# Performance work log

Measured on AMD Instinct MI355X. Metric: run time of the kernel, lower is better.

## Reference

```python
import jax, jax.numpy as jnp
import numpy as np

DIM = 384
HEADS = 8
ADLA = 343
HWD = 14
N = HWD ** 3
B = 8
HEAD_DIM = DIM // HEADS
SCALE = HEAD_DIM ** -0.5
POOL = 7  # ceil(343**(1/3)); 14 is evenly divisible by 7


def _lin_mat(in_size, out_size):
    # PyTorch trilinear interpolation (align_corners=False), one axis -> (out,in) matrix
    scale = in_size / out_size
    x = (np.arange(out_size) + 0.5) * scale - 0.5
    x = np.clip(x, 0.0, in_size - 1)
    x0 = np.floor(x).astype(np.int64)
    x1 = np.minimum(x0 + 1, in_size - 1)
    w = (x - x0).astype(np.float32)
    M = np.zeros((out_size, in_size), np.float32)
    M[np.arange(out_size), x0] += 1.0 - w
    M[np.arange(out_size), x1] += w
    return jnp.asarray(M)


def _interp3(t, out_hwd):
    # t: (..., a, b, c) -> (..., H, W, D) trilinear, align_corners=False
    Ma = _lin_mat(t.shape[-3], out_hwd[0])
    Mb = _lin_mat(t.shape[-2], out_hwd[1])
    Mc = _lin_mat(t.shape[-1], out_hwd[2])
    return jnp.einsum('...abc,xa,yb,zc->...xyz', t, Ma, Mb, Mc)


def setup_inputs() -> dict:
    key = jax.random.key(0)
    ks = jax.random.split(key, 16)
    std = 0.02
    return {
        'x': jax.random.normal(ks[0], (B, N, DIM), jnp.float32),
        'Wq': jax.random.normal(ks[1], (DIM, DIM), jnp.float32) * std,
        'Wkv': jax.random.normal(ks[2], (DIM, 2 * DIM), jnp.float32) * std,
        'Wproj': jax.random.normal(ks[3], (DIM, DIM), jnp.float32) * std,
        'bproj': jnp.zeros((DIM,), jnp.float32),
        'dwc_w': jax.random.normal(ks[4], (DIM, 1, 3, 3, 3), jnp.float32) * std,
        'dwc_b': jnp.zeros((DIM,), jnp.float32),
        'an_bias': jax.random.normal(ks[5], (HEADS, ADLA, 7, 7, 7), jnp.float32) * std,
        'na_bias': jax.random.normal(ks[6], (HEADS, ADLA, 7, 7, 7), jnp.float32) * std,
        'ah_bias': jax.random.normal(ks[7], (1, HEADS, ADLA, HWD, 1, 1), jnp.float32) * std,
        'aw_bias': jax.random.normal(ks[8], (1, HEADS, ADLA, 1, HWD, 1), jnp.float32) * std,
        'ad_bias': jax.random.normal(ks[9], (1, HEADS, ADLA, 1, 1, HWD), jnp.float32) * std,
        'ha_bias': jax.random.normal(ks[10], (1, HEADS, HWD, 1, 1, ADLA), jnp.float32) * std,
        'wa_bias': jax.random.normal(ks[11], (1, HEADS, 1, HWD, 1, ADLA), jnp.float32) * std,
        'da_bias': jax.random.normal(ks[12], (1, HEADS, 1, 1, HWD, ADLA), jnp.float32) * std,
        'H': HWD, 'W': HWD, 'D': HWD,
    }


def reference(x, Wq, Wkv, Wproj, bproj, dwc_w, dwc_b, an_bias, na_bias,
              ah_bias, aw_bias, ad_bias, ha_bias, wa_bias, da_bias, H, W, D):
    b, n, c = x.shape
    h, hd = HEADS, c // HEADS
    q = x @ Wq                       # (b, n, c)
    kv = x @ Wkv                     # (b, n, 2c)  (sr_ratio == 1)
    k, v = kv[..., :c], kv[..., c:]
    # AdaptiveAvgPool3d 14->7: even 2x2x2 block mean; spatial flatten order matches torch
    adla = q.reshape(b, POOL, H // POOL, POOL, W // POOL, POOL, D // POOL, c)
    adla = adla.mean(axis=(2, 4, 6)).reshape(b, ADLA, c)   # (b, A, c)
    qh = q.reshape(b, n, h, hd).transpose(0, 2, 1, 3)       # (b,h,n,hd)
    kh = k.reshape(b, n, h, hd).transpose(0, 2, 1, 3)
    vh = v.reshape(b, n, h, hd).transpose(0, 2, 1, 3)
    ath = adla.reshape(b, ADLA, h, hd).transpose(0, 2, 1, 3)  # (b,h,A,hd)
    # stage 1: anchor -> tokens
    pb1 = _interp3(an_bias, (H, W, D)).reshape(1, h, ADLA, n)
    pb2 = (ah_bias + aw_bias + ad_bias).reshape(1, h, ADLA, n)
    logits1 = jnp.einsum('bhad,bhnd->bhan', ath * SCALE, kh) + pb1 + pb2
    adla_v = jnp.einsum('bhan,bhnd->bhad', jax.nn.softmax(logits1, axis=-1), vh)
    # stage 2: tokens -> anchor
    ab1 = _interp3(na_bias, (H, W, D)).reshape(1, h, ADLA, n).transpose(0, 1, 3, 2)
    ab2 = (ha_bias + wa_bias + da_bias).reshape(1, h, n, ADLA)
    logits2 = jnp.einsum('bhnd,bhad->bhna', qh * SCALE, ath) + ab1 + ab2
    out = jnp.einsum('bhna,bhad->bhnd', jax.nn.softmax(logits2, axis=-1), adla_v)
    out = out.transpose(0, 2, 1, 3).reshape(b, n, c)
    # depthwise Conv3d on v volume, fused into residual
    vvol = v.reshape(b, H, W, D, c).transpose(0, 4, 1, 2, 3)  # (b,c,H,W,D)
    dwc = jax.lax.conv_general_dilated(
        vvol, dwc_w, (1, 1, 1), 'SAME',
        dimension_numbers=('NCDHW', 'OIDHW', 'NCDHW'), feature_group_count=c)
    dwc = dwc + dwc_b[None, :, None, None, None]
    out = out + dwc.transpose(0, 2, 3, 4, 1).reshape(b, n, c)
    return out @ Wproj + bproj
```

## Files before the change

kernel.cpp:

```cpp
#include <hip/hip_runtime.h>
#include <hip/hip_bf16.h>
#include <cstdint>

typedef __bf16 bf16;
typedef __attribute__((ext_vector_type(8))) __bf16 bf16x8;
typedef __attribute__((ext_vector_type(4))) __bf16 bf16x4;
typedef __attribute__((ext_vector_type(2))) __bf16 bf16x2;
typedef __attribute__((ext_vector_type(4))) float f32x4;

constexpr int DIM = 384;
constexpr int HEAD_DIM = 48;
constexpr int ADLA_N = 343;
constexpr int NTOK = 2744;
constexpr int BATCH = 8;
constexpr int MTOT = BATCH * NTOK;
constexpr float SCALE = 0.14433756729740643f;
constexpr int B1W = 2816;
constexpr int B2W = 384;
constexpr int ADV_W = 352;
constexpr int SEG = 6;

__global__ void transpose_weights(const float* __restrict__ Wq,
                                  const float* __restrict__ Wkv,
                                  const float* __restrict__ Wproj,
                                  bf16* __restrict__ WTall,
                                  bf16* __restrict__ WprojT) {
  int idx = blockIdx.x * 256 + threadIdx.x;
  const int total1 = 1152 * 384;
  if (idx < total1) {
    int j = idx / 384, k = idx % 384;
    WTall[idx] = (bf16)((j < 384) ? Wq[k * 384 + j] : Wkv[k * 768 + (j - 384)]);
  } else {
    int i2 = idx - total1;
    if (i2 < 384 * 384) {
      int j = i2 / 384, k = i2 % 384;
      WprojT[i2] = (bf16)Wproj[k * 384 + j];
    }
  }
}

__device__ __forceinline__ void lin_w(int i, int& i0, int& i1, float& w) {
  float f = 0.5f * (float)i - 0.25f;
  f = fminf(fmaxf(f, 0.0f), 6.0f);
  i0 = (int)f;
  w = f - (float)i0;
  i1 = (i0 + 1 < 7) ? i0 + 1 : 6;
}

__device__ __forceinline__ float interp3(const float* __restrict__ p, int x, int y, int z) {
  int x0, x1, y0, y1, z0, z1; float wx, wy, wz;
  lin_w(x, x0, x1, wx); lin_w(y, y0, y1, wy); lin_w(z, z0, z1, wz);
  float c000 = p[x0*49 + y0*7 + z0], c001 = p[x0*49 + y0*7 + z1];
  float c010 = p[x0*49 + y1*7 + z0], c011 = p[x0*49 + y1*7 + z1];
  float c100 = p[x1*49 + y0*7 + z0], c101 = p[x1*49 + y0*7 + z1];
  float c110 = p[x1*49 + y1*7 + z0], c111 = p[x1*49 + y1*7 + z1];
  float c00 = c000 + wz * (c001 - c000), c01 = c010 + wz * (c011 - c010);
  float c10 = c100 + wz * (c101 - c100), c11 = c110 + wz * (c111 - c110);
  float c0 = c00 + wy * (c01 - c00), c1 = c10 + wy * (c11 - c10);
  return c0 + wx * (c1 - c0);
}

__global__ void bias1_kernel(const float* __restrict__ an, const float* __restrict__ ah,
                             const float* __restrict__ aw, const float* __restrict__ ad,
                             bf16* __restrict__ out) {
  int h = blockIdx.x / ADLA_N, a = blockIdx.x % ADLA_N;
  const float* anp = an + ((size_t)h * ADLA_N + a) * 343;
  const float* ahp = ah + ((size_t)h * ADLA_N + a) * 14;
  const float* awp = aw + ((size_t)h * ADLA_N + a) * 14;
  const float* adp = ad + ((size_t)h * ADLA_N + a) * 14;
  bf16* op = out + ((size_t)h * ADLA_N + a) * B1W;
  for (int n = threadIdx.x; n < B1W; n += 256) {
    if (n < NTOK) {
      int x = n / 196, y = (n / 14) % 14, z = n % 14;
      float v = interp3(anp, x, y, z) + ahp[x] + awp[y] + adp[z];
      op[n] = (bf16)v;
    } else {
      op[n] = (bf16)0.f;
    }
  }
}

__global__ __launch_bounds__(256)
void bias2_kernel(const float* __restrict__ na, const float* __restrict__ ha,
                  const float* __restrict__ wa, const float* __restrict__ da,
                  bf16* __restrict__ out) {
  __shared__ bf16 t[64 * 66];
  const int tid = threadIdx.x;
  const int wv = tid >> 6, lane = tid & 63;
  const int n0 = blockIdx.x * 64, a0 = blockIdx.y * 64;
  const int h = blockIdx.z;
  const int nc = min(n0 + lane, NTOK - 1);
  const int x = nc / 196, y = (nc / 14) % 14, z = nc % 14;
  int x0, x1, y0, y1, z0, z1; float wx, wy, wz;
  lin_w(x, x0, x1, wx); lin_w(y, y0, y1, wy); lin_w(z, z0, z1, wz);
  const int o[8] = { x0*49 + y0*7 + z0, x0*49 + y0*7 + z1,
                     x0*49 + y1*7 + z0, x0*49 + y1*7 + z1,
                     x1*49 + y0*7 + z0, x1*49 + y0*7 + z1,
                     x1*49 + y1*7 + z0, x1*49 + y1*7 + z1 };
  const float wgt[8] = { (1.f-wx)*(1.f-wy)*(1.f-wz), (1.f-wx)*(1.f-wy)*wz,
                         (1.f-wx)*wy*(1.f-wz),       (1.f-wx)*wy*wz,
                         wx*(1.f-wy)*(1.f-wz),       wx*(1.f-wy)*wz,
                         wx*wy*(1.f-wz),             wx*wy*wz };
#pragma unroll
  for (int j = 0; j < 16; j++) {
    const int al = wv * 16 + j;
    const int a = a0 + al;
    float s = 0.f;
    if (a < ADLA_N) {
      const float* p = na + ((size_t)h * ADLA_N + a) * 343;
#pragma unroll
      for (int k = 0; k < 8; k++) s += p[o[k]] * wgt[k];
      s += ha[((size_t)h * 14 + x) * ADLA_N + a]
         + wa[((size_t)h * 14 + y) * ADLA_N + a]
         + da[((size_t)h * 14 + z) * ADLA_N + a];
    }
    t[lane * 66 + al] = (bf16)s;
  }
  __syncthreads();
#pragma unroll
  for (int j = 0; j < 16; j++) {
    const int nr = wv * 16 + j;
    if (n0 + nr < NTOK)
      out[((size_t)h * NTOK + n0 + nr) * B2W + a0 + lane] = t[nr * 66 + lane];
  }
}

template <int MODE, typename AT, typename OT>
__global__ __launch_bounds__(256)
void gemm128(const AT* __restrict__ A, const bf16* __restrict__ BT, int M,
             OT* __restrict__ O0, bf16* __restrict__ O1, bf16* __restrict__ O2,
             const float* __restrict__ bias) {
  __shared__ __align__(16) bf16 As[128 * 40];
  __shared__ __align__(16) bf16 Bs[128 * 40];
  const int tid = threadIdx.x;
  const int wv = tid >> 6, lane = tid & 63;
  const int m0 = blockIdx.x * 128, n0 = blockIdx.y * 128;
  const int wr = wv >> 1, wc = wv & 1;
  f32x4 zero4 = {0.f, 0.f, 0.f, 0.f};
  f32x4 acc[4][4];
#pragma unroll
  for (int i = 0; i < 4; i++)
#pragma unroll
    for (int j = 0; j < 4; j++) acc[i][j] = zero4;

  for (int k0 = 0; k0 < 384; k0 += 32) {
    __syncthreads();
#pragma unroll
    for (int i = 0; i < 2; i++) {
      int flat = i * 256 + tid;
      int row = flat >> 2, cg = flat & 3;
      int gr = m0 + row; if (gr >= M) gr = M - 1;
      bf16x8 av;
      if constexpr (sizeof(AT) == 4) {
        const float4* s4 = (const float4*)(A + (size_t)gr * 384 + k0 + cg * 8);
        float4 a = s4[0], b = s4[1];
        av[0]=(bf16)a.x; av[1]=(bf16)a.y; av[2]=(bf16)a.z; av[3]=(bf16)a.w;
        av[4]=(bf16)b.x; av[5]=(bf16)b.y; av[6]=(bf16)b.z; av[7]=(bf16)b.w;
      } else {
        av = *(const bf16x8*)(A + (size_t)gr * 384 + k0 + cg * 8);
      }
      *(bf16x8*)(As + row * 40 + cg * 8) = av;
      int nr = n0 + row;
      *(bf16x8*)(Bs + row * 40 + cg * 8) = *(const bf16x8*)(BT + (size_t)nr * 384 + k0 + cg * 8);
    }
    __syncthreads();
    bf16x8 af[4], bfr[4];
#pragma unroll
    for (int t = 0; t < 4; t++) {
      af[t]  = *(const bf16x8*)(As + (wr * 64 + t * 16 + (lane & 15)) * 40 + (lane >> 4) * 8);
      bfr[t] = *(const bf16x8*)(Bs + (wc * 64 + t * 16 + (lane & 15)) * 40 + (lane >> 4) * 8);
    }
#pragma unroll
    for (int rt = 0; rt < 4; rt++)
#pragma unroll
      for (int ct = 0; ct < 4; ct++)
        acc[rt][ct] = __builtin_amdgcn_mfma_f32_16x16x32_bf16(af[rt], bfr[ct], acc[rt][ct], 0, 0, 0);
  }
  const int quad = lane >> 4, colL = lane & 15;
#pragma unroll
  for (int rt = 0; rt < 4; rt++) {
#pragma unroll
    for (int ct = 0; ct < 4; ct++) {
      int gcol = n0 + wc * 64 + ct * 16 + colL;
#pragma unroll
      for (int r = 0; r < 4; r++) {
        int grow = m0 + wr * 64 + rt * 16 + quad * 4 + r;
        if (grow < M) {
          float v = acc[rt][ct][r];
          if (MODE == 1) {
            v += bias[gcol];
            O0[(size_t)grow * 384 + gcol] = (OT)v;
          } else {
            bf16* dst; int c;
            if (gcol < 384)      { dst = (bf16*)O0; c = gcol; }
            else if (gcol < 768) { dst = O1; c = gcol - 384; }
            else                 { dst = O2; c = gcol - 768; }
            dst[(size_t)grow * 384 + c] = (bf16)v;
          }
        }
      }
    }
  }
}

__global__ void transpose_v(const bf16* __restrict__ v, bf16* __restrict__ vT) {
  __shared__ bf16 t[64][65];
  int n0 = blockIdx.x * 64, c0 = blockIdx.y * 64, b = blockIdx.z;
  int tid = threadIdx.x;
  int cl = tid & 63, rs = tid >> 6;
  for (int j = 0; j < 16; j++) {
    int r = rs * 16 + j;
    int n = n0 + r;
    if (n < NTOK) t[cl][r] = v[((size_t)b * NTOK + n) * DIM + c0 + cl];
  }
  __syncthreads();
  int nl = tid & 63, cs = tid >> 6;
  int n = n0 + nl;
  if (n < NTOK)
    for (int j = 0; j < 16; j++) {
      int cc = cs * 16 + j;
      vT[((size_t)b * DIM + c0 + cc) * NTOK + n] = t[cc][nl];
    }
}

__global__ void pool_kernel(const bf16* __restrict__ q, bf16* __restrict__ adla) {
  int idx = blockIdx.x * 256 + threadIdx.x;
  if (idx >= BATCH * ADLA_N * DIM) return;
  int c = idx % DIM;
  int a = (idx / DIM) % ADLA_N;
  int b = idx / (DIM * ADLA_N);
  int a0 = a / 49, a1 = (a / 7) % 7, a2 = a % 7;
  float s = 0.f;
#pragma unroll
  for (int i = 0; i < 2; i++)
#pragma unroll
    for (int j = 0; j < 2; j++)
#pragma unroll
      for (int k = 0; k < 2; k++) {
        int n = (a0 * 2 + i) * 196 + (a1 * 2 + j) * 14 + (a2 * 2 + k);
        s += (float)q[((size_t)b * NTOK + n) * DIM + c];
      }
  adla[idx] = (bf16)(s * 0.125f);
}

template <int MODE>
__global__ __launch_bounds__(256)
void attn_kernel(const bf16* __restrict__ Amat, const bf16* __restrict__ Kmat,
                 const bf16* __restrict__ Vt, const bf16* __restrict__ Bias,
                 bf16* __restrict__ Out, float* __restrict__ OutP,
                 float* __restrict__ RsP,
                 int AR, int NC, int biasW,
                 size_t vtB, size_t vtH, int vtS) {
  __shared__ __align__(16) bf16 kT[128 * 64];
  __shared__ __align__(16) bf16 vTs[48 * 128];
  __shared__ __align__(16) bf16 pT[64 * 128];
  const int tid = threadIdx.x;
  const int wv = tid >> 6, lane = tid & 63;

  int h, bI, rblk, seg;
  {
    const int id = blockIdx.x;
    h = id & 7;
    int t = id >> 3;
    if (MODE == 0) { rblk = t % 6; t /= 6; bI = t & 7; seg = t >> 3; }
    else           { bI = t & 7; rblk = t >> 3; seg = 0; }
  }
  const int bh = bI * 8 + h;
  const int r0 = rblk * 64;
  const int quad = lane >> 4, colL = lane & 15;
  const int rowL = wv * 16 + colL;

  int ar = r0 + rowL; if (ar >= AR) ar = AR - 1;
  const bf16* aRow = Amat + ((size_t)bI * AR + ar) * DIM + h * HEAD_DIM;
  bf16x8 af0 = *(const bf16x8*)(aRow + quad * 8);
  bf16x8 af1;
#pragma unroll
  for (int e = 0; e < 8; e++) af1[e] = (bf16)0.f;
  if (quad < 2) af1 = *(const bf16x8*)(aRow + 32 + quad * 8);

  f32x4 zero4 = {0.f, 0.f, 0.f, 0.f};
  f32x4 acc[3] = {zero4, zero4, zero4};
  float rowsum = 0.f;
  const int nCh = (NC + 127) >> 7;
  const int ch0 = seg * 4;
  const int ch1 = min(nCh, ch0 + 4);
  int br = r0 + rowL; if (br >= AR) br = AR - 1;
  const bf16* biasRow = Bias + ((size_t)h * AR + br) * biasW + quad * 4;

  bf16x8 kreg[4], vreg[3];
  auto load_tile = [&](int ch) {
    const int c0 = ch << 7;
#pragma unroll
    for (int i = 0; i < 4; i++) {
      int flat = i * 256 + tid;
      int row = flat >> 3, cg = flat & 7;
      int kg = (cg < 6) ? cg : 0;
      int gr = c0 + row; if (gr >= NC) gr = NC - 1;
      kreg[i] = *(const bf16x8*)(Kmat + ((size_t)bI * NC + gr) * DIM + h * HEAD_DIM + kg * 8);
    }
#pragma unroll
    for (int i = 0; i < 3; i++) {
      int flat = i * 256 + tid;
      int d = flat >> 4, cg = flat & 15;
      int cc = c0 + cg * 8; if (cc > vtS - 8) cc = vtS - 8;
      vreg[i] = *(const bf16x8*)(Vt + (size_t)bI * vtB + (size_t)h * vtH + (size_t)d * vtS + cc);
    }
  };
  auto write_tile = [&]() {
#pragma unroll
    for (int i = 0; i < 4; i++) {
      int flat = i * 256 + tid;
      int row = flat >> 3, cg = flat & 7;
      *(bf16x8*)(kT + row * 64 + ((cg ^ (row & 7)) << 3)) = kreg[i];
    }
#pragma unroll
    for (int i = 0; i < 3; i++) {
      int flat = i * 256 + tid;
      int d = flat >> 4, cg = flat & 15;
      *(bf16x8*)(vTs + d * 128 + ((cg ^ (d & 15)) << 3)) = vreg[i];
    }
  };

  load_tile(ch0);
  write_tile();
  __syncthreads();

  for (int ch = ch0; ch < ch1; ch++) {
    const int c0 = ch << 7;
    const bool hasNext = (ch + 1 < ch1);
    if (hasNext) load_tile(ch + 1);

    bf16x4 bv[8];
#pragma unroll
    for (int ct = 0; ct < 8; ct++)
      bv[ct] = *(const bf16x4*)(biasRow + c0 + ct * 16);

    f32x4 sacc[8];
#pragma unroll
    for (int ct = 0; ct < 8; ct++) sacc[ct] = zero4;
#pragma unroll
    for (int ct = 0; ct < 8; ct++) {
      int krow = ct * 16 + colL;
      bf16x8 b0 = *(const bf16x8*)(kT + krow * 64 + ((quad ^ (krow & 7)) << 3));
      bf16x8 b1 = *(const bf16x8*)(kT + krow * 64 + (((4 | quad) ^ (krow & 7)) << 3));
      sacc[ct] = __builtin_amdgcn_mfma_f32_16x16x32_bf16(b0, af0, sacc[ct], 0, 0, 0);
      sacc[ct] = __builtin_amdgcn_mfma_f32_16x16x32_bf16(b1, af1, sacc[ct], 0, 0, 0);
    }
#pragma unroll
    for (int ct = 0; ct < 8; ct++) {
      int cbase = c0 + ct * 16 + quad * 4;
      bf16x4 pw;
#pragma unroll
      for (int j = 0; j < 4; j++) {
        float s = sacc[ct][j] * SCALE + (float)bv[ct][j];
        s = fminf(fmaxf(s, -60.f), 60.f);
        float p = ((cbase + j) < NC) ? __expf(s) : 0.f;
        rowsum += p;
        pw[j] = (bf16)p;
      }
      int cg = ct * 2 + (quad >> 1);
      *(bf16x4*)(pT + rowL * 128 + ((cg ^ (rowL & 15)) << 3) + (quad & 1) * 4) = pw;
    }
#pragma unroll
    for (int ks = 0; ks < 4; ks++) {
      bf16x8 pf = *(const bf16x8*)(pT + rowL * 128 + (((ks * 4 + quad) ^ (rowL & 15)) << 3));
#pragma unroll
      for (int dt = 0; dt < 3; dt++) {
        const int vrow = dt * 16 + colL;
        bf16x8 vf = *(const bf16x8*)(vTs + vrow * 128 + (((ks * 4 + quad) ^ (vrow & 15)) << 3));
        acc[dt] = __builtin_amdgcn_mfma_f32_16x16x32_bf16(pf, vf, acc[dt], 0, 0, 0);
      }
    }
    __syncthreads();
    if (hasNext) {
      write_tile();
      __syncthreads();
    }
  }

  rowsum += __shfl_xor(rowsum, 16, 64);
  rowsum += __shfl_xor(rowsum, 32, 64);

  if (MODE == 0) {
#pragma unroll
    for (int dt = 0; dt < 3; dt++)
#pragma unroll
      for (int r = 0; r < 4; r++) {
        int a = r0 + wv * 16 + quad * 4 + r;
        size_t rowD = ((size_t)seg * 64 + bh) * 48 + dt * 16 + colL;
        if (a < AR)
          OutP[rowD * ADV_W + a] = acc[dt][r];
        else if (a < ADV_W)
          OutP[rowD * ADV_W + a] = 0.f;
      }
    if (quad == 0) {
      int a = r0 + rowL;
      if (a < AR)
        RsP[((size_t)seg * 64 + bh) * ADV_W + a] = rowsum;
    }
  } else {
    float inv[4];
#pragma unroll
    for (int r = 0; r < 4; r++) inv[r] = 1.f / __shfl(rowsum, quad * 4 + r, 64);
#pragma unroll
    for (int dt = 0; dt < 3; dt++)
#pragma unroll
      for (int r = 0; r < 4; r++) {
        int n = r0 + wv * 16 + quad * 4 + r;
        if (n < AR)
          Out[((size_t)bI * AR + n) * DIM + h * HEAD_DIM + dt * 16 + colL] = (bf16)(acc[dt][r] * inv[r]);
      }
  }
}

__global__ void attn1_reduce(const float* __restrict__ advP, const float* __restrict__ rsP,
                             bf16* __restrict__ advT) {
  int idx = blockIdx.x * 256 + threadIdx.x;
  if (idx >= 64 * 48 * ADV_W) return;
  int a = idx % ADV_W;
  int d = (idx / ADV_W) % 48;
  int bh = idx / (ADV_W * 48);
  if (a >= ADLA_N) { advT[idx] = (bf16)0.f; return; }
  float s = 0.f, rs = 0.f;
#pragma unroll
  for (int g = 0; g < SEG; g++) {
    s  += advP[(((size_t)g * 64 + bh) * 48 + d) * ADV_W + a];
    rs += rsP[((size_t)g * 64 + bh) * ADV_W + a];
  }
  advT[((size_t)bh * 48 + d) * ADV_W + a] = (bf16)(s / rs);
}

__global__ __launch_bounds__(256)
void dwc_kernel(const bf16* __restrict__ v, const float* __restrict__ w,
                const float* __restrict__ bias, bf16* __restrict__ io) {
  __shared__ float wts[128 * 27];
  const int tid = threadIdx.x;
  const int cg = blockIdx.y;
  const int b  = blockIdx.z;
  for (int i = tid; i < 128 * 27; i += 256)
    wts[i] = w[(size_t)cg * 128 * 27 + i];
  __syncthreads();

  const int wv = tid >> 6, lane = tid & 63;
  const int xy = blockIdx.x * 4 + wv;
  const int x = xy / 14, y = xy % 14;
  const int c0 = lane * 2;
  const int cglob = cg * 128 + c0;
  const bf16* vb_ = v + (size_t)b * NTOK * DIM + cglob;
  bf16* iob = io + (size_t)b * NTOK * DIM + cglob + (size_t)(x * 196 + y * 14) * DIM;

  float2 acc[14];
#pragma unroll
  for (int z = 0; z < 14; z++) acc[z] = make_float2(0.f, 0.f);

#pragma unroll
  for (int dx = -1; dx <= 1; dx++) {
    int X = x + dx; if ((unsigned)X >= 14u) continue;
#pragma unroll
    for (int dy = -1; dy <= 1; dy++) {
      int Y = y + dy; if ((unsigned)Y >= 14u) continue;
      const bf16* colp = vb_ + (size_t)(X * 196 + Y * 14) * DIM;
      float2 col[14];
#pragma unroll
      for (int z = 0; z < 14; z++) {
        bf16x2 u = *(const bf16x2*)(colp + (size_t)z * DIM);
        col[z] = make_float2((float)u[0], (float)u[1]);
      }
      const int tb = (dx + 1) * 9 + (dy + 1) * 3;
      const float w0a = wts[c0 * 27 + tb],     w0b = wts[(c0 + 1) * 27 + tb];
      const float w1a = wts[c0 * 27 + tb + 1], w1b = wts[(c0 + 1) * 27 + tb + 1];
      const float w2a = wts[c0 * 27 + tb + 2], w2b = wts[(c0 + 1) * 27 + tb + 2];
#pragma unroll
      for (int z = 0; z < 14; z++) {
        float2 s = acc[z];
        if (z > 0)  { s.x += col[z - 1].x * w0a; s.y += col[z - 1].y * w0b; }
        s.x += col[z].x * w1a; s.y += col[z].y * w1b;
        if (z < 13) { s.x += col[z + 1].x * w2a; s.y += col[z + 1].y * w2b; }
        acc[z] = s;
      }
    }
  }

  const float bsa = bias[cglob], bsb = bias[cglob + 1];
#pragma unroll
  for (int z = 0; z < 14; z++) {
    bf16x2 u = *(const bf16x2*)(iob + (size_t)z * DIM);
    bf16x2 o;
    o[0] = (bf16)((float)u[0] + acc[z].x + bsa);
    o[1] = (bf16)((float)u[1] + acc[z].y + bsb);
    *(bf16x2*)(iob + (size_t)z * DIM) = o;
  }
}

extern "C" void kernel_launch(void* const* d_in, const int* in_sizes, int n_in,
                              void* d_out, int out_size, void* d_ws, size_t ws_size,
                              hipStream_t stream) {
  const float* x     = (const float*)d_in[0];
  const float* Wq    = (const float*)d_in[1];
  const float* Wkv   = (const float*)d_in[2];
  const float* Wproj = (const float*)d_in[3];
  const float* bproj = (const float*)d_in[4];
  const float* dwcw  = (const float*)d_in[5];
  const float* dwcb  = (const float*)d_in[6];
  const float* an    = (const float*)d_in[7];
  const float* na    = (const float*)d_in[8];
  const float* ahb   = (const float*)d_in[9];
  const float* awb   = (const float*)d_in[10];
  const float* adb   = (const float*)d_in[11];
  const float* hab   = (const float*)d_in[12];
  const float* wab   = (const float*)d_in[13];
  const float* dab   = (const float*)d_in[14];
  float* out = (float*)d_out;

  uint8_t* ws = (uint8_t*)d_ws;
  size_t off = 0;
  auto carveB = [&](size_t bytes) -> void* {
    void* p = ws + off;
    off += ((bytes + 255) & ~(size_t)255);
    return p;
  };
  auto carve = [&](size_t elems) -> bf16* { return (bf16*)carveB(elems * 2); };
  bf16*  wtall  = carve((size_t)1152 * 384);
  bf16*  wprojT = carve((size_t)384 * 384);
  bf16*  qb     = carve((size_t)MTOT * 384 + 128);
  bf16*  kb     = carve((size_t)MTOT * 384 + 128);
  bf16*  vb     = carve((size_t)MTOT * 384 + 128);
  bf16*  vTb    = carve((size_t)MTOT * 384 + 128);
  bf16*  adla   = carve((size_t)BATCH * ADLA_N * 384 + 128);
  bf16*  advT   = carve((size_t)64 * 48 * ADV_W + 128);
  bf16*  bias1  = carve((size_t)8 * ADLA_N * B1W);
  float* advP   = (float*)carveB((size_t)SEG * 64 * 48 * ADV_W * 4);
  float* rsP    = (float*)carveB((size_t)SEG * 64 * ADV_W * 4);
  bf16*  bias2  = kb;
  bf16*  aout   = vTb;

  transpose_weights<<<dim3((1152 * 384 + 384 * 384 + 255) / 256), 256, 0, stream>>>(
      Wq, Wkv, Wproj, wtall, wprojT);
  bias1_kernel<<<dim3(8 * ADLA_N), 256, 0, stream>>>(an, ahb, awb, adb, bias1);
  gemm128<0, float, bf16><<<dim3(172, 9), 256, 0, stream>>>(
      x, wtall, MTOT, qb, kb, vb, nullptr);
  transpose_v<<<dim3(43, 6, 8), 256, 0, stream>>>(vb, vTb);
  pool_kernel<<<dim3((BATCH * ADLA_N * DIM + 255) / 256), 256, 0, stream>>>(qb, adla);
  attn_kernel<0><<<dim3(6 * 64 * SEG), 256, 0, stream>>>(
      adla, kb, vTb, bias1, nullptr, advP, rsP,
      ADLA_N, NTOK, B1W, (size_t)384 * NTOK, (size_t)48 * NTOK, NTOK);
  attn1_reduce<<<dim3((64 * 48 * ADV_W + 255) / 256), 256, 0, stream>>>(advP, rsP, advT);
  bias2_kernel<<<dim3(43, 6, 8), 256, 0, stream>>>(na, hab, wab, dab, bias2);
  attn_kernel<1><<<dim3(43 * 64), 256, 0, stream>>>(
      qb, adla, advT, bias2, aout, nullptr, nullptr,
      NTOK, ADLA_N, B2W, (size_t)8 * 48 * ADV_W, (size_t)48 * ADV_W, ADV_W);
  dwc_kernel<<<dim3(49, 3, 8), 256, 0, stream>>>(vb, dwcw, dwcb, aout);
  gemm128<1, bf16, float><<<dim3(172, 3), 256, 0, stream>>>(
      aout, wprojT, MTOT, out, nullptr, nullptr, bproj);
}
```

Before: 425.6 us.

## Double-buffer attention tiles in LDS with 64-column chunks and higher occupancy

```diff
diff --git a/kernel.cpp b/kernel.cpp
--- a/kernel.cpp
+++ b/kernel.cpp
@@ -244,16 +244,16 @@
 }
 
 template <int MODE>
-__global__ __launch_bounds__(256)
+__global__ __launch_bounds__(256, 4)
 void attn_kernel(const bf16* __restrict__ Amat, const bf16* __restrict__ Kmat,
                  const bf16* __restrict__ Vt, const bf16* __restrict__ Bias,
                  bf16* __restrict__ Out, float* __restrict__ OutP,
                  float* __restrict__ RsP,
                  int AR, int NC, int biasW,
                  size_t vtB, size_t vtH, int vtS) {
-  __shared__ __align__(16) bf16 kT[128 * 64];
-  __shared__ __align__(16) bf16 vTs[48 * 128];
-  __shared__ __align__(16) bf16 pT[64 * 128];
+  __shared__ __align__(16) bf16 kT[2][64 * 64];
+  __shared__ __align__(16) bf16 vTs[2][48 * 64];
+  __shared__ __align__(16) bf16 pT[64 * 64];
   const int tid = threadIdx.x;
   const int wv = tid >> 6, lane = tid & 63;
 
@@ -281,17 +281,17 @@
   f32x4 zero4 = {0.f, 0.f, 0.f, 0.f};
   f32x4 acc[3] = {zero4, zero4, zero4};
   float rowsum = 0.f;
-  const int nCh = (NC + 127) >> 7;
-  const int ch0 = seg * 4;
-  const int ch1 = min(nCh, ch0 + 4);
+  const int nCh = (NC + 63) >> 6;
+  const int ch0 = (MODE == 0) ? seg * 8 : 0;
+  const int ch1 = (MODE == 0) ? min(nCh, ch0 + 8) : nCh;
   int br = r0 + rowL; if (br >= AR) br = AR - 1;
   const bf16* biasRow = Bias + ((size_t)h * AR + br) * biasW + quad * 4;
 
-  bf16x8 kreg[4], vreg[3];
+  bf16x8 kreg[2], vreg[2];
   auto load_tile = [&](int ch) {
-    const int c0 = ch << 7;
-#pragma unroll
-    for (int i = 0; i < 4; i++) {
+    const int c0 = ch << 6;
+#pragma unroll
+    for (int i = 0; i < 2; i++) {
       int flat = i * 256 + tid;
       int row = flat >> 3, cg = flat & 7;
       int kg = (cg < 6) ? cg : 0;
@@ -299,55 +299,63 @@
       kreg[i] = *(const bf16x8*)(Kmat + ((size_t)bI * NC + gr) * DIM + h * HEAD_DIM + kg * 8);
     }
 #pragma unroll
-    for (int i = 0; i < 3; i++) {
+    for (int i = 0; i < 2; i++) {
       int flat = i * 256 + tid;
-      int d = flat >> 4, cg = flat & 15;
+      int d = flat >> 3; if (d > 47) d = 47;
+      int cg = flat & 7;
       int cc = c0 + cg * 8; if (cc > vtS - 8) cc = vtS - 8;
       vreg[i] = *(const bf16x8*)(Vt + (size_t)bI * vtB + (size_t)h * vtH + (size_t)d * vtS + cc);
     }
   };
-  auto write_tile = [&]() {
-#pragma unroll
-    for (int i = 0; i < 4; i++) {
+  auto write_tile = [&](int buf) {
+    bf16* kd = kT[buf];
+    bf16* vd = vTs[buf];
+#pragma unroll
+    for (int i = 0; i < 2; i++) {
       int flat = i * 256 + tid;
       int row = flat >> 3, cg = flat & 7;
-      *(bf16x8*)(kT + row * 64 + ((cg ^ (row & 7)) << 3)) = kreg[i];
-    }
-#pragma unroll
-    for (int i = 0; i < 3; i++) {
+      *(bf16x8*)(kd + row * 64 + ((cg ^ (row & 7)) << 3)) = kreg[i];
+    }
+#pragma unroll
+    for (int i = 0; i < 2; i++) {
       int flat = i * 256 + tid;
-      int d = flat >> 4, cg = flat & 15;
-      *(bf16x8*)(vTs + d * 128 + ((cg ^ (d & 15)) << 3)) = vreg[i];
+      int d = flat >> 3; if (d > 47) d = 47;
+      int cg = flat & 7;
+      *(bf16x8*)(vd + d * 64 + ((cg ^ (d & 7)) << 3)) = vreg[i];
     }
   };
 
   load_tile(ch0);
-  write_tile();
+  write_tile(0);
   __syncthreads();
+  int cur = 0;
 
   for (int ch = ch0; ch < ch1; ch++) {
-    const int c0 = ch << 7;
+    const int c0 = ch << 6;
     const bool hasNext = (ch + 1 < ch1);
     if (hasNext) load_tile(ch + 1);
 
-    bf16x4 bv[8];
-#pragma unroll
-    for (int ct = 0; ct < 8; ct++)
+    bf16x4 bv[4];
+#pragma unroll
+    for (int ct = 0; ct < 4; ct++)
       bv[ct] = *(const bf16x4*)(biasRow + c0 + ct * 16);
 
-    f32x4 sacc[8];
-#pragma unroll
-    for (int ct = 0; ct < 8; ct++) sacc[ct] = zero4;
-#pragma unroll
-    for (int ct = 0; ct < 8; ct++) {
+    const bf16* kc = kT[cur];
+    const bf16* vc = vTs[cur];
+
+    f32x4 sacc[4];
+#pragma unroll
+    for (int ct = 0; ct < 4; ct++) sacc[ct] = zero4;
+#pragma unroll
+    for (int ct = 0; ct < 4; ct++) {
       int krow = ct * 16 + colL;
-      bf16x8 b0 = *(const bf16x8*)(kT + krow * 64 + ((quad ^ (krow & 7)) << 3));
-      bf16x8 b1 = *(const bf16x8*)(kT + krow * 64 + (((4 | quad) ^ (krow & 7)) << 3));
+      bf16x8 b0 = *(const bf16x8*)(kc + krow * 64 + ((quad ^ (krow & 7)) << 3));
+      bf16x8 b1 = *(const bf16x8*)(kc + krow * 64 + (((4 | quad) ^ (krow & 7)) << 3));
       sacc[ct] = __builtin_amdgcn_mfma_f32_16x16x32_bf16(b0, af0, sacc[ct], 0, 0, 0);
       sacc[ct] = __builtin_amdgcn_mfma_f32_16x16x32_bf16(b1, af1, sacc[ct], 0, 0, 0);
     }
 #pragma unroll
-    for (int ct = 0; ct < 8; ct++) {
+    for (int ct = 0; ct < 4; ct++) {
       int cbase = c0 + ct * 16 + quad * 4;
       bf16x4 pw;
 #pragma unroll
@@ -358,24 +366,22 @@
         rowsum += p;
         pw[j] = (bf16)p;
       }
-      int cg = ct * 2 + (quad >> 1);
-      *(bf16x4*)(pT + rowL * 128 + ((cg ^ (rowL & 15)) << 3) + (quad & 1) * 4) = pw;
-    }
-#pragma unroll
-    for (int ks = 0; ks < 4; ks++) {
-      bf16x8 pf = *(const bf16x8*)(pT + rowL * 128 + (((ks * 4 + quad) ^ (rowL & 15)) << 3));
+      int g = ct * 2 + (quad >> 1);
+      *(bf16x4*)(pT + rowL * 64 + ((g ^ (rowL & 7)) << 3) + (quad & 1) * 4) = pw;
+    }
+#pragma unroll
+    for (int ks = 0; ks < 2; ks++) {
+      bf16x8 pf = *(const bf16x8*)(pT + rowL * 64 + (((ks * 4 + quad) ^ (rowL & 7)) << 3));
 #pragma unroll
       for (int dt = 0; dt < 3; dt++) {
         const int vrow = dt * 16 + colL;
-        bf16x8 vf = *(const bf16x8*)(vTs + vrow * 128 + (((ks * 4 + quad) ^ (vrow & 15)) << 3));
+        bf16x8 vf = *(const bf16x8*)(vc + vrow * 64 + (((ks * 4 + quad) ^ (vrow & 7)) << 3));
         acc[dt] = __builtin_amdgcn_mfma_f32_16x16x32_bf16(pf, vf, acc[dt], 0, 0, 0);
       }
     }
+    if (hasNext) write_tile(cur ^ 1);
     __syncthreads();
-    if (hasNext) {
-      write_tile();
-      __syncthreads();
-    }
+    cur ^= 1;
   }
 
   rowsum += __shfl_xor(rowsum, 16, 64);
```

Result: no change. 421.9 us (-0.9%).
